# Performance work log

Hardware: AMD Instinct MI355X
Metric: run time of the kernel (lower is better)

The kernel has to match this reference:

```python
import jax, jax.numpy as jnp
import numpy as np

N, E, D, H, L, G, OUT = 100000, 1600000, 64, 64, 3, 128, 10
BN_EPS = 1e-5

def setup_inputs() -> dict:
    key = jax.random.key(0)
    ks = jax.random.split(key, 8)
    x = jax.random.normal(ks[0], (N, D), dtype=jnp.float32)
    edge_index = jax.random.randint(ks[1], (2, E), 0, N, dtype=jnp.int64)
    batch = jnp.sort(jax.random.randint(ks[2], (N,), 0, G, dtype=jnp.int64))
    W1 = jax.random.normal(ks[3], (L, D, H), dtype=jnp.float32) / np.sqrt(D)
    b1 = jnp.zeros((L, H), dtype=jnp.float32)
    gamma = jnp.ones((L, H), dtype=jnp.float32)
    beta = jnp.zeros((L, H), dtype=jnp.float32)
    W2 = jax.random.normal(ks[4], (L, H, H), dtype=jnp.float32) / np.sqrt(H)
    b2 = jnp.zeros((L, H), dtype=jnp.float32)
    Wout = jax.random.normal(ks[5], (L, H, OUT), dtype=jnp.float32) / np.sqrt(H)
    bout = jnp.zeros((L, OUT), dtype=jnp.float32)
    return {"x": x, "edge_index": edge_index, "batch": batch, "W1": W1, "b1": b1,
            "gamma": gamma, "beta": beta, "W2": W2, "b2": b2, "Wout": Wout, "bout": bout}

def _gin_layer(x, src, dst, W1, b1, g, bt, W2, b2):
    # GIN sum aggregation, eps = 0: (1+eps)*x + sum_{j->i} x_j
    agg = x + jax.ops.segment_sum(x[src], dst, num_segments=x.shape[0])
    h = agg @ W1 + b1
    mu = jnp.mean(h, axis=0)
    var = jnp.var(h, axis=0)
    h = (h - mu) * jax.lax.rsqrt(var + BN_EPS) * g + bt  # BatchNorm1d (batch stats)
    h = jax.nn.relu(h)
    return h @ W2 + b2

def reference(x, edge_index, batch, W1, b1, gamma, beta, W2, b2, Wout, bout):
    src, dst = edge_index[0], edge_index[1]
    score = jnp.zeros((G, OUT), dtype=x.dtype)
    for l in range(L):
        x = _gin_layer(x, src, dst, W1[l], b1[l], gamma[l], beta[l], W2[l], b2[l])
        pooled = jax.ops.segment_sum(x, batch, num_segments=G)  # global_add_pool
        score = score + (pooled @ Wout[l] + bout[l])  # dropout is identity in eval
    return score
```

## Files before the change

kernel.cpp:

```cpp
#include <hip/hip_runtime.h>

typedef unsigned int uint;

#define N_NODES 100000
#define E_EDGES 1600000
#define L_LAYERS 3
#define G_GRAPHS 128
#define OUT_F 10
#define BN_EPS 1e-5f

#define BSHIFT 7
#define NSTRIPE ((N_NODES + 127) >> 7)
#define CHUNK 2048
#define NCHUNK ((E_EDGES + CHUNK - 1) / CHUNK)
#define PAD8(d) (((d) + 7) & ~7)
#define BCAP (2048 * 103)
#define FB_GRID (103 * 8)
#define SCAP 2560
#define SNBR 3584

__device__ __forceinline__ uint bf_pack(float a, float b) {
    uint ua = __float_as_uint(a);
    ua = (ua + 0x7fffu + ((ua >> 16) & 1u)) >> 16;
    uint ub = __float_as_uint(b);
    ub = (ub + 0x7fffu + ((ub >> 16) & 1u)) >> 16;
    return ua | (ub << 16);
}
__device__ __forceinline__ unsigned short bf1(float a) {
    uint ua = __float_as_uint(a);
    return (unsigned short)((ua + 0x7fffu + ((ua >> 16) & 1u)) >> 16);
}
__device__ __forceinline__ float lo16(uint u) { return __uint_as_float(u << 16); }
__device__ __forceinline__ float hi16(uint u) { return __uint_as_float(u & 0xffff0000u); }

__global__ __launch_bounds__(256) void init_kernel(int* __restrict__ gcur,
                                                   int* __restrict__ scur) {
    int t = blockIdx.x * 256 + threadIdx.x;
    if (t < 8) gcur[t] = t * BCAP;
    if (t < NSTRIPE) scur[t] = t * SCAP;
}

__global__ __launch_bounds__(256) void fillA_kernel(
    const int* __restrict__ src, const int* __restrict__ dst,
    int* __restrict__ gcur, int2* __restrict__ epair) {
    __shared__ int lcnt[8];
    __shared__ int lbase[8];
    int tid = threadIdx.x;
    int base = blockIdx.x * CHUNK;
    if (tid < 8) lcnt[tid] = 0;
    __syncthreads();

    int sd[8], ss[8], bk[8], off[8];
    #pragma unroll
    for (int it = 0; it < 8; ++it) {
        int e = base + it * 256 + tid;
        bk[it] = -1;
        if (e < E_EDGES) {
            sd[it] = dst[e];
            ss[it] = src[e];
            bk[it] = (sd[it] >> BSHIFT) & 7;
            off[it] = atomicAdd(&lcnt[bk[it]], 1);
        }
    }
    __syncthreads();
    if (tid < 8) lbase[tid] = atomicAdd(&gcur[tid], lcnt[tid]);
    __syncthreads();
    #pragma unroll
    for (int it = 0; it < 8; ++it) {
        if (bk[it] >= 0)
            epair[lbase[bk[it]] + off[it]] = make_int2(ss[it], sd[it]);
    }
}

__global__ __launch_bounds__(256) void fillB2_kernel(
    const int2* __restrict__ epair1, const int* __restrict__ gcur,
    int* __restrict__ scur, int2* __restrict__ epair2) {
    __shared__ int lcnt[98];
    __shared__ int lbase[98];
    int tid = threadIdx.x;
    int g = blockIdx.x & 7;
    int c = blockIdx.x >> 3;
    int ebeg = g * BCAP + c * CHUNK;
    int eend = gcur[g];
    if (tid < 98) lcnt[tid] = 0;
    __syncthreads();

    int2 pp[8]; int bk[8], off[8];
    #pragma unroll
    for (int it = 0; it < 8; ++it) {
        int i = ebeg + it * 256 + tid;
        bk[it] = -1;
        if (i < eend) {
            pp[it] = epair1[i];
            bk[it] = pp[it].y >> 10;
            off[it] = atomicAdd(&lcnt[bk[it]], 1);
        }
    }
    __syncthreads();
    if (tid < 98 && lcnt[tid] > 0)
        lbase[tid] = atomicAdd(&scur[(tid << 3) | g], lcnt[tid]);
    __syncthreads();
    #pragma unroll
    for (int it = 0; it < 8; ++it) {
        if (bk[it] >= 0)
            epair2[lbase[bk[it]] + off[it]] = pp[it];
    }
}

__global__ __launch_bounds__(256) void fillC2_kernel(
    const int2* __restrict__ epair2, const int* __restrict__ scur,
    int* __restrict__ rbeg, int* __restrict__ rend, int* __restrict__ nbr) {
    __shared__ int cnt[128];
    __shared__ int loc[128];
    __shared__ int off[128];
    __shared__ int buf[SNBR];
    __shared__ int stotal;
    int s = blockIdx.x;
    int tid = threadIdx.x;
    int node0 = s << 7;
    int qbeg = s * SCAP;
    int qend = scur[s];
    if (tid < 128) cnt[tid] = 0;
    __syncthreads();

    for (int i = qbeg + tid; i < qend; i += 256)
        atomicAdd(&cnt[epair2[i].y & 127], 1);
    __syncthreads();

    int v = (tid < 128) ? PAD8(cnt[tid]) : 0;
    if (tid < 128) loc[tid] = v;
    __syncthreads();
    for (int o = 1; o < 128; o <<= 1) {
        int u = (tid < 128 && tid >= o) ? loc[tid - o] : 0;
        __syncthreads();
        if (tid < 128) loc[tid] += u;
        __syncthreads();
    }
    int sbase = s * SNBR;
    if (tid < 128) {
        int ex = loc[tid] - v;
        off[tid] = ex;
        int node = node0 + tid;
        if (node < N_NODES) {
            rbeg[node] = sbase + ex;
            rend[node] = sbase + ex + v;
        }
    }
    if (tid == 0) stotal = loc[127];
    __syncthreads();
    int total = stotal;

    for (int i = tid; i < total; i += 256) buf[i] = N_NODES;
    __syncthreads();

    for (int i = qbeg + tid; i < qend; i += 256) {
        int2 p = epair2[i];
        int pos = atomicAdd(&off[p.y & 127], 1);
        buf[pos] = p.x;
    }
    __syncthreads();

    for (int i = tid * 4; i < total; i += 1024)
        *reinterpret_cast<int4*>(nbr + sbase + i) = *reinterpret_cast<const int4*>(buf + i);
}

__global__ __launch_bounds__(256) void tobf_kernel(const float* __restrict__ x,
                                                   uint* __restrict__ xbf) {
    int i = blockIdx.x * 256 + threadIdx.x;
    if (i < N_NODES * 8) {
        float4 a = reinterpret_cast<const float4*>(x)[i * 2];
        float4 b = reinterpret_cast<const float4*>(x)[i * 2 + 1];
        uint4 o;
        o.x = bf_pack(a.x, a.y);
        o.y = bf_pack(a.z, a.w);
        o.z = bf_pack(b.x, b.y);
        o.w = bf_pack(b.z, b.w);
        reinterpret_cast<uint4*>(xbf)[i] = o;
    }
    if (i < 8) reinterpret_cast<uint4*>(xbf)[N_NODES * 8 + i] = make_uint4(0, 0, 0, 0);
}

__global__ __launch_bounds__(256) void gemm1_fused_kernel(
    const uint* __restrict__ xbf, const int* __restrict__ rbeg,
    const int* __restrict__ rend, const int* __restrict__ nbr,
    const float* __restrict__ W1, const float* __restrict__ b1,
    unsigned short* __restrict__ h16, float* __restrict__ stats) {
    __shared__ float sA[64][68];
    __shared__ unsigned short sWh[64][64];
    int tid = threadIdx.x;
    int row0 = blockIdx.x * 64;

    for (int i = tid; i < 1024; i += 256) {
        float4 w = reinterpret_cast<const float4*>(W1)[i];
        unsigned short* p = &sWh[0][0] + i * 4;
        p[0] = bf1(w.x); p[1] = bf1(w.y); p[2] = bf1(w.z); p[3] = bf1(w.w);
    }

    const uint4* xb4 = reinterpret_cast<const uint4*>(xbf);
    int c8 = tid & 7;
    int rslot = tid >> 3;
    for (int rr = 0; rr < 2; ++rr) {
        int r = rslot + 32 * rr;
        int gr = row0 + r;
        float a0 = 0.f, a1 = 0.f, a2 = 0.f, a3 = 0.f;
        float a4 = 0.f, a5 = 0.f, a6 = 0.f, a7 = 0.f;
        if (gr < N_NODES) {
            uint4 sv = xb4[(size_t)gr * 8 + c8];
            a0 = lo16(sv.x); a1 = hi16(sv.x); a2 = lo16(sv.y); a3 = hi16(sv.y);
            a4 = lo16(sv.z); a5 = hi16(sv.z); a6 = lo16(sv.w); a7 = hi16(sv.w);
            int beg = rbeg[gr], end = rend[gr];
            int4 ia = *reinterpret_cast<const int4*>(nbr + beg);
            int4 ib = *reinterpret_cast<const int4*>(nbr + beg + 4);
            for (int j = beg; j < end; j += 8) {
                int4 ian = *reinterpret_cast<const int4*>(nbr + j + 8);
                int4 ibn = *reinterpret_cast<const int4*>(nbr + j + 12);
                uint4 v0 = xb4[(size_t)ia.x * 8 + c8];
                uint4 v1 = xb4[(size_t)ia.y * 8 + c8];
                uint4 v2 = xb4[(size_t)ia.z * 8 + c8];
                uint4 v3 = xb4[(size_t)ia.w * 8 + c8];
                uint4 v4 = xb4[(size_t)ib.x * 8 + c8];
                uint4 v5 = xb4[(size_t)ib.y * 8 + c8];
                uint4 v6 = xb4[(size_t)ib.z * 8 + c8];
                uint4 v7 = xb4[(size_t)ib.w * 8 + c8];
                a0 += lo16(v0.x); a1 += hi16(v0.x); a2 += lo16(v0.y); a3 += hi16(v0.y);
                a4 += lo16(v0.z); a5 += hi16(v0.z); a6 += lo16(v0.w); a7 += hi16(v0.w);
                a0 += lo16(v1.x); a1 += hi16(v1.x); a2 += lo16(v1.y); a3 += hi16(v1.y);
                a4 += lo16(v1.z); a5 += hi16(v1.z); a6 += lo16(v1.w); a7 += hi16(v1.w);
                a0 += lo16(v2.x); a1 += hi16(v2.x); a2 += lo16(v2.y); a3 += hi16(v2.y);
                a4 += lo16(v2.z); a5 += hi16(v2.z); a6 += lo16(v2.w); a7 += hi16(v2.w);
                a0 += lo16(v3.x); a1 += hi16(v3.x); a2 += lo16(v3.y); a3 += hi16(v3.y);
                a4 += lo16(v3.z); a5 += hi16(v3.z); a6 += lo16(v3.w); a7 += hi16(v3.w);
                a0 += lo16(v4.x); a1 += hi16(v4.x); a2 += lo16(v4.y); a3 += hi16(v4.y);
                a4 += lo16(v4.z); a5 += hi16(v4.z); a6 += lo16(v4.w); a7 += hi16(v4.w);
                a0 += lo16(v5.x); a1 += hi16(v5.x); a2 += lo16(v5.y); a3 += hi16(v5.y);
                a4 += lo16(v5.z); a5 += hi16(v5.z); a6 += lo16(v5.w); a7 += hi16(v5.w);
                a0 += lo16(v6.x); a1 += hi16(v6.x); a2 += lo16(v6.y); a3 += hi16(v6.y);
                a4 += lo16(v6.z); a5 += hi16(v6.z); a6 += lo16(v6.w); a7 += hi16(v6.w);
                a0 += lo16(v7.x); a1 += hi16(v7.x); a2 += lo16(v7.y); a3 += hi16(v7.y);
                a4 += lo16(v7.z); a5 += hi16(v7.z); a6 += lo16(v7.w); a7 += hi16(v7.w);
                ia = ian; ib = ibn;
            }
        }
        *reinterpret_cast<float4*>(&sA[r][c8 * 8])     = make_float4(a0, a1, a2, a3);
        *reinterpret_cast<float4*>(&sA[r][c8 * 8 + 4]) = make_float4(a4, a5, a6, a7);
    }
    __syncthreads();

    int ct = tid & 15, rt = tid >> 4;
    int cbase = ct * 4, rbase = rt * 4;
    float4 bias = reinterpret_cast<const float4*>(b1)[ct];
    float acc[4][4];
    #pragma unroll
    for (int i = 0; i < 4; ++i) {
        acc[i][0] = bias.x; acc[i][1] = bias.y; acc[i][2] = bias.z; acc[i][3] = bias.w;
    }
    for (int k = 0; k < 64; ++k) {
        float A0 = sA[rbase + 0][k], A1 = sA[rbase + 1][k];
        float A2 = sA[rbase + 2][k], A3 = sA[rbase + 3][k];
        uint2 wp = *reinterpret_cast<const uint2*>(&sWh[k][cbase]);
        float w0 = lo16(wp.x), w1 = hi16(wp.x), w2 = lo16(wp.y), w3 = hi16(wp.y);
        acc[0][0] = fmaf(A0, w0, acc[0][0]); acc[0][1] = fmaf(A0, w1, acc[0][1]);
        acc[0][2] = fmaf(A0, w2, acc[0][2]); acc[0][3] = fmaf(A0, w3, acc[0][3]);
        acc[1][0] = fmaf(A1, w0, acc[1][0]); acc[1][1] = fmaf(A1, w1, acc[1][1]);
        acc[1][2] = fmaf(A1, w2, acc[1][2]); acc[1][3] = fmaf(A1, w3, acc[1][3]);
        acc[2][0] = fmaf(A2, w0, acc[2][0]); acc[2][1] = fmaf(A2, w1, acc[2][1]);
        acc[2][2] = fmaf(A2, w2, acc[2][2]); acc[2][3] = fmaf(A2, w3, acc[2][3]);
        acc[3][0] = fmaf(A3, w0, acc[3][0]); acc[3][1] = fmaf(A3, w1, acc[3][1]);
        acc[3][2] = fmaf(A3, w2, acc[3][2]); acc[3][3] = fmaf(A3, w3, acc[3][3]);
    }

    float csum[4] = {0.f, 0.f, 0.f, 0.f};
    float csq[4]  = {0.f, 0.f, 0.f, 0.f};
    #pragma unroll
    for (int i = 0; i < 4; ++i) {
        int gr = row0 + rbase + i;
        if (gr < N_NODES) {
            uint2 o;
            o.x = bf_pack(acc[i][0], acc[i][1]);
            o.y = bf_pack(acc[i][2], acc[i][3]);
            *reinterpret_cast<uint2*>(&h16[(size_t)gr * 64 + cbase]) = o;
            #pragma unroll
            for (int j = 0; j < 4; ++j) {
                csum[j] += acc[i][j];
                csq[j]  += acc[i][j] * acc[i][j];
            }
        }
    }
    __syncthreads();
    float* scratch = &sA[0][0];
    #pragma unroll
    for (int j = 0; j < 4; ++j) {
        scratch[rt * 136 + cbase + j]      = csum[j];
        scratch[rt * 136 + 64 + cbase + j] = csq[j];
    }
    __syncthreads();
    if (tid < 64) {
        float s = 0.f, q = 0.f;
        #pragma unroll
        for (int r2 = 0; r2 < 16; ++r2) {
            s += scratch[r2 * 136 + tid];
            q += scratch[r2 * 136 + 64 + tid];
        }
        unsafeAtomicAdd(&stats[tid], s);
        unsafeAtomicAdd(&stats[64 + tid], q);
    }
}

__global__ __launch_bounds__(256) void gemm2_pool_kernel(
    const unsigned short* __restrict__ h16, const float* __restrict__ stats,
    const float* __restrict__ gamma, const float* __restrict__ beta,
    const float* __restrict__ W2, const float* __restrict__ b2,
    const int* __restrict__ batch, float* __restrict__ pooled,
    unsigned short* __restrict__ xout) {
    __shared__ float sA[64][68];
    __shared__ unsigned short sWh[64][64];
    int tid = threadIdx.x;
    int row0 = blockIdx.x * 64;

    for (int i = tid; i < 1024; i += 256) {
        float4 w = reinterpret_cast<const float4*>(W2)[i];
        unsigned short* p = &sWh[0][0] + i * 4;
        p[0] = bf1(w.x); p[1] = bf1(w.y); p[2] = bf1(w.z); p[3] = bf1(w.w);
    }

    int c8 = tid & 7;
    float scv[8], shv[8];
    #pragma unroll
    for (int k = 0; k < 8; ++k) {
        int col = c8 * 8 + k;
        float mu = stats[col] * (1.0f / N_NODES);
        float var = stats[64 + col] * (1.0f / N_NODES) - mu * mu;
        scv[k] = gamma[col] * rsqrtf(var + BN_EPS);
        shv[k] = beta[col] - mu * scv[k];
    }

    const uint4* h4 = reinterpret_cast<const uint4*>(h16);
    for (int i = tid; i < 512; i += 256) {
        int r = i >> 3;
        int gr = row0 + r;
        float o[8] = {0.f, 0.f, 0.f, 0.f, 0.f, 0.f, 0.f, 0.f};
        if (gr < N_NODES) {
            uint4 v = h4[(size_t)gr * 8 + c8];
            float f[8] = {lo16(v.x), hi16(v.x), lo16(v.y), hi16(v.y),
                          lo16(v.z), hi16(v.z), lo16(v.w), hi16(v.w)};
            #pragma unroll
            for (int k = 0; k < 8; ++k)
                o[k] = fmaxf(fmaf(f[k], scv[k], shv[k]), 0.f);
        }
        *reinterpret_cast<float4*>(&sA[r][c8 * 8]) = make_float4(o[0], o[1], o[2], o[3]);
        *reinterpret_cast<float4*>(&sA[r][c8 * 8 + 4]) = make_float4(o[4], o[5], o[6], o[7]);
    }
    __syncthreads();

    int ct = tid & 15, rt = tid >> 4;
    int cbase = ct * 4, rbase = rt * 4;
    float4 bias = reinterpret_cast<const float4*>(b2)[ct];
    float acc[4][4];
    #pragma unroll
    for (int i = 0; i < 4; ++i) {
        acc[i][0] = bias.x; acc[i][1] = bias.y; acc[i][2] = bias.z; acc[i][3] = bias.w;
    }
    for (int k = 0; k < 64; ++k) {
        float A0 = sA[rbase + 0][k], A1 = sA[rbase + 1][k];
        float A2 = sA[rbase + 2][k], A3 = sA[rbase + 3][k];
        uint2 wp = *reinterpret_cast<const uint2*>(&sWh[k][cbase]);
        float w0 = lo16(wp.x), w1 = hi16(wp.x), w2 = lo16(wp.y), w3 = hi16(wp.y);
        acc[0][0] = fmaf(A0, w0, acc[0][0]); acc[0][1] = fmaf(A0, w1, acc[0][1]);
        acc[0][2] = fmaf(A0, w2, acc[0][2]); acc[0][3] = fmaf(A0, w3, acc[0][3]);
        acc[1][0] = fmaf(A1, w0, acc[1][0]); acc[1][1] = fmaf(A1, w1, acc[1][1]);
        acc[1][2] = fmaf(A1, w2, acc[1][2]); acc[1][3] = fmaf(A1, w3, acc[1][3]);
        acc[2][0] = fmaf(A2, w0, acc[2][0]); acc[2][1] = fmaf(A2, w1, acc[2][1]);
        acc[2][2] = fmaf(A2, w2, acc[2][2]); acc[2][3] = fmaf(A2, w3, acc[2][3]);
        acc[3][0] = fmaf(A3, w0, acc[3][0]); acc[3][1] = fmaf(A3, w1, acc[3][1]);
        acc[3][2] = fmaf(A3, w2, acc[3][2]); acc[3][3] = fmaf(A3, w3, acc[3][3]);
    }

    #pragma unroll
    for (int i = 0; i < 4; ++i) {
        int gr = row0 + rbase + i;
        if (gr < N_NODES) {
            uint2 o;
            o.x = bf_pack(acc[i][0], acc[i][1]);
            o.y = bf_pack(acc[i][2], acc[i][3]);
            *reinterpret_cast<uint2*>(&xout[(size_t)gr * 64 + cbase]) = o;
        }
    }

    int lastrow = row0 + 63; if (lastrow >= N_NODES) lastrow = N_NODES - 1;
    int b0 = batch[row0], bL = batch[lastrow];
    if (b0 == bL) {
        float psum[4] = {0.f, 0.f, 0.f, 0.f};
        #pragma unroll
        for (int i = 0; i < 4; ++i) {
            int gr = row0 + rbase + i;
            if (gr < N_NODES) {
                #pragma unroll
                for (int j = 0; j < 4; ++j) psum[j] += acc[i][j];
            }
        }
        __syncthreads();
        float* scratch = &sA[0][0];
        #pragma unroll
        for (int j = 0; j < 4; ++j) scratch[rt * 68 + cbase + j] = psum[j];
        __syncthreads();
        if (tid < 64) {
            float s = 0.f;
            #pragma unroll
            for (int r2 = 0; r2 < 16; ++r2) s += scratch[r2 * 68 + tid];
            unsafeAtomicAdd(&pooled[b0 * 64 + tid], s);
        }
    } else {
        #pragma unroll
        for (int j = 0; j < 4; ++j) {
            float pacc = 0.f;
            int curb = -1;
            #pragma unroll
            for (int i = 0; i < 4; ++i) {
                int gr = row0 + rbase + i;
                if (gr < N_NODES) {
                    int b = batch[gr];
                    if (b != curb) {
                        if (curb >= 0) unsafeAtomicAdd(&pooled[curb * 64 + cbase + j], pacc);
                        curb = b;
                        pacc = 0.f;
                    }
                    pacc += acc[i][j];
                }
            }
            if (curb >= 0) unsafeAtomicAdd(&pooled[curb * 64 + cbase + j], pacc);
        }
    }
}

__global__ void out_kernel(const float* __restrict__ pooled,
                           const float* __restrict__ Wout,
                           const float* __restrict__ bout,
                           float* __restrict__ score) {
    int idx = blockIdx.x * blockDim.x + threadIdx.x;
    if (idx >= G_GRAPHS * OUT_F) return;
    int g = idx / OUT_F;
    int o = idx - g * OUT_F;
    float acc = bout[o];
    #pragma unroll
    for (int k = 0; k < 64; ++k) acc += pooled[g * 64 + k] * Wout[k * OUT_F + o];
    score[idx] += acc;
}

extern "C" void kernel_launch(void* const* d_in, const int* in_sizes, int n_in,
                              void* d_out, int out_size, void* d_ws, size_t ws_size,
                              hipStream_t stream) {
    const float* x     = (const float*)d_in[0];
    const int*   ei    = (const int*)d_in[1];
    const int*   batch = (const int*)d_in[2];
    const float* W1    = (const float*)d_in[3];
    const float* b1    = (const float*)d_in[4];
    const float* gamma = (const float*)d_in[5];
    const float* beta  = (const float*)d_in[6];
    const float* W2    = (const float*)d_in[7];
    const float* b2    = (const float*)d_in[8];
    const float* Wout  = (const float*)d_in[9];
    const float* bout  = (const float*)d_in[10];
    float* out = (float*)d_out;

    unsigned short* H16 = (unsigned short*)d_ws;
    uint*  XBF    = (uint*)(H16 + (size_t)N_NODES * 64);
    float* stats  = (float*)(XBF + (size_t)(N_NODES + 1) * 32);
    float* pooled = stats + 128;
    int*   gcur   = (int*)(pooled + (size_t)G_GRAPHS * 64);
    int*   scur   = gcur + 8;
    int*   rbeg   = scur + 784;
    int*   rend   = rbeg + N_NODES;
    int*   nbr    = rend + N_NODES;
    int2*  epair1 = (int2*)(nbr + (size_t)NSTRIPE * SNBR + 16);
    int2*  epair2 = epair1 + (size_t)8 * BCAP;

    const int* src = ei;
    const int* dst = ei + E_EDGES;

    (void)hipMemsetAsync(d_out, 0, (size_t)G_GRAPHS * OUT_F * sizeof(float), stream);

    init_kernel<<<(NSTRIPE + 255) / 256, 256, 0, stream>>>(gcur, scur);
    fillA_kernel<<<NCHUNK, 256, 0, stream>>>(src, dst, gcur, epair1);
    fillB2_kernel<<<FB_GRID, 256, 0, stream>>>(epair1, gcur, scur, epair2);
    fillC2_kernel<<<NSTRIPE, 256, 0, stream>>>(epair2, scur, rbeg, rend, nbr);
    tobf_kernel<<<(N_NODES * 8 + 255) / 256, 256, 0, stream>>>(x, XBF);

    int nb = (N_NODES + 63) / 64;

    for (int l = 0; l < L_LAYERS; ++l) {
        (void)hipMemsetAsync(stats, 0, (128 + (size_t)G_GRAPHS * 64) * sizeof(float), stream);

        gemm1_fused_kernel<<<nb, 256, 0, stream>>>(XBF, rbeg, rend, nbr,
            W1 + l * 64 * 64, b1 + l * 64, H16, stats);
        gemm2_pool_kernel<<<nb, 256, 0, stream>>>(H16, stats,
            gamma + l * 64, beta + l * 64, W2 + l * 64 * 64, b2 + l * 64, batch,
            pooled, (unsigned short*)XBF);
        out_kernel<<<(G_GRAPHS * OUT_F + 127) / 128, 128, 0, stream>>>(
            pooled, Wout + l * 64 * OUT_F, bout + l * OUT_F, out);
    }
}
```

Measured before the change: 355.1 us.

## Use bf16 MFMA for the dense 64x64 GEMMs in gemm1 and gemm2 kernels

Replaces the scalar FMA 4x4 register-tiled GEMM in both fused kernels with __builtin_amdgcn_mfma_f32_16x16x32_bf16. The A tile is now stored as bf16 in shared memory and the weights are stored transposed so each wave can load 8-element k fragments. The epilogues (bf16 stores, batchnorm statistics, pooling atomics) are remapped to the MFMA output layout. This cuts ALU time for the GEMM phase and shrinks LDS use, but it rounds the aggregated activations to bf16 before the multiply and the output stores become 2-byte scattered writes.

```diff
diff --git a/kernel.cpp b/kernel.cpp
--- a/kernel.cpp
+++ b/kernel.cpp
@@ -1,6 +1,8 @@
 #include <hip/hip_runtime.h>
 
 typedef unsigned int uint;
+typedef short bf16x8 __attribute__((ext_vector_type(8)));
+typedef float f32x4 __attribute__((ext_vector_type(4)));
 
 #define N_NODES 100000
 #define E_EDGES 1600000
@@ -185,15 +187,18 @@
     const int* __restrict__ rend, const int* __restrict__ nbr,
     const float* __restrict__ W1, const float* __restrict__ b1,
     unsigned short* __restrict__ h16, float* __restrict__ stats) {
-    __shared__ float sA[64][68];
-    __shared__ unsigned short sWh[64][64];
+    __shared__ unsigned short sA[64][72];
+    __shared__ unsigned short sW[64][72];
     int tid = threadIdx.x;
     int row0 = blockIdx.x * 64;
 
     for (int i = tid; i < 1024; i += 256) {
+        int k = i >> 4, cb = (i & 15) * 4;
         float4 w = reinterpret_cast<const float4*>(W1)[i];
-        unsigned short* p = &sWh[0][0] + i * 4;
-        p[0] = bf1(w.x); p[1] = bf1(w.y); p[2] = bf1(w.z); p[3] = bf1(w.w);
+        sW[cb + 0][k] = bf1(w.x);
+        sW[cb + 1][k] = bf1(w.y);
+        sW[cb + 2][k] = bf1(w.z);
+        sW[cb + 3][k] = bf1(w.w);
     }
 
     const uint4* xb4 = reinterpret_cast<const uint4*>(xbf);
@@ -241,65 +246,63 @@
                 ia = ian; ib = ibn;
             }
         }
-        *reinterpret_cast<float4*>(&sA[r][c8 * 8])     = make_float4(a0, a1, a2, a3);
-        *reinterpret_cast<float4*>(&sA[r][c8 * 8 + 4]) = make_float4(a4, a5, a6, a7);
-    }
-    __syncthreads();
-
-    int ct = tid & 15, rt = tid >> 4;
-    int cbase = ct * 4, rbase = rt * 4;
-    float4 bias = reinterpret_cast<const float4*>(b1)[ct];
-    float acc[4][4];
-    #pragma unroll
-    for (int i = 0; i < 4; ++i) {
-        acc[i][0] = bias.x; acc[i][1] = bias.y; acc[i][2] = bias.z; acc[i][3] = bias.w;
-    }
-    for (int k = 0; k < 64; ++k) {
-        float A0 = sA[rbase + 0][k], A1 = sA[rbase + 1][k];
-        float A2 = sA[rbase + 2][k], A3 = sA[rbase + 3][k];
-        uint2 wp = *reinterpret_cast<const uint2*>(&sWh[k][cbase]);
-        float w0 = lo16(wp.x), w1 = hi16(wp.x), w2 = lo16(wp.y), w3 = hi16(wp.y);
-        acc[0][0] = fmaf(A0, w0, acc[0][0]); acc[0][1] = fmaf(A0, w1, acc[0][1]);
-        acc[0][2] = fmaf(A0, w2, acc[0][2]); acc[0][3] = fmaf(A0, w3, acc[0][3]);
-        acc[1][0] = fmaf(A1, w0, acc[1][0]); acc[1][1] = fmaf(A1, w1, acc[1][1]);
-        acc[1][2] = fmaf(A1, w2, acc[1][2]); acc[1][3] = fmaf(A1, w3, acc[1][3]);
-        acc[2][0] = fmaf(A2, w0, acc[2][0]); acc[2][1] = fmaf(A2, w1, acc[2][1]);
-        acc[2][2] = fmaf(A2, w2, acc[2][2]); acc[2][3] = fmaf(A2, w3, acc[2][3]);
-        acc[3][0] = fmaf(A3, w0, acc[3][0]); acc[3][1] = fmaf(A3, w1, acc[3][1]);
-        acc[3][2] = fmaf(A3, w2, acc[3][2]); acc[3][3] = fmaf(A3, w3, acc[3][3]);
-    }
-
-    float csum[4] = {0.f, 0.f, 0.f, 0.f};
-    float csq[4]  = {0.f, 0.f, 0.f, 0.f};
-    #pragma unroll
-    for (int i = 0; i < 4; ++i) {
-        int gr = row0 + rbase + i;
-        if (gr < N_NODES) {
-            uint2 o;
-            o.x = bf_pack(acc[i][0], acc[i][1]);
-            o.y = bf_pack(acc[i][2], acc[i][3]);
-            *reinterpret_cast<uint2*>(&h16[(size_t)gr * 64 + cbase]) = o;
-            #pragma unroll
-            for (int j = 0; j < 4; ++j) {
-                csum[j] += acc[i][j];
-                csq[j]  += acc[i][j] * acc[i][j];
+        uint4 o;
+        o.x = bf_pack(a0, a1); o.y = bf_pack(a2, a3);
+        o.z = bf_pack(a4, a5); o.w = bf_pack(a6, a7);
+        *reinterpret_cast<uint4*>(&sA[r][c8 * 8]) = o;
+    }
+    __syncthreads();
+
+    int w = tid >> 6;
+    int l = tid & 63;
+    int lr = l & 15;
+    int lk = l >> 4;
+    f32x4 acc[4];
+    #pragma unroll
+    for (int ct = 0; ct < 4; ++ct) {
+        float b = b1[ct * 16 + lr];
+        acc[ct] = (f32x4){b, b, b, b};
+    }
+    #pragma unroll
+    for (int ct = 0; ct < 4; ++ct) {
+        #pragma unroll
+        for (int kc = 0; kc < 2; ++kc) {
+            bf16x8 av = *reinterpret_cast<const bf16x8*>(&sA[w * 16 + lr][kc * 32 + lk * 8]);
+            bf16x8 bv = *reinterpret_cast<const bf16x8*>(&sW[ct * 16 + lr][kc * 32 + lk * 8]);
+            acc[ct] = __builtin_amdgcn_mfma_f32_16x16x32_bf16(av, bv, acc[ct], 0, 0, 0);
+        }
+    }
+
+    float s4[4] = {0.f, 0.f, 0.f, 0.f};
+    float q4[4] = {0.f, 0.f, 0.f, 0.f};
+    #pragma unroll
+    for (int ct = 0; ct < 4; ++ct) {
+        #pragma unroll
+        for (int r = 0; r < 4; ++r) {
+            int row = row0 + w * 16 + lk * 4 + r;
+            float v = acc[ct][r];
+            if (row < N_NODES) {
+                h16[(size_t)row * 64 + ct * 16 + lr] = bf1(v);
+                s4[ct] += v;
+                q4[ct] += v * v;
             }
         }
     }
     __syncthreads();
-    float* scratch = &sA[0][0];
-    #pragma unroll
-    for (int j = 0; j < 4; ++j) {
-        scratch[rt * 136 + cbase + j]      = csum[j];
-        scratch[rt * 136 + 64 + cbase + j] = csq[j];
+    float* scr = reinterpret_cast<float*>(&sW[0][0]);
+    int g16 = w * 4 + lk;
+    #pragma unroll
+    for (int ct = 0; ct < 4; ++ct) {
+        scr[g16 * 64 + ct * 16 + lr] = s4[ct];
+        scr[1024 + g16 * 64 + ct * 16 + lr] = q4[ct];
     }
     __syncthreads();
     if (tid < 64) {
         float s = 0.f, q = 0.f;
         #pragma unroll
         for (int r2 = 0; r2 < 16; ++r2) {
-            s += scratch[r2 * 136 + tid];
-            q += scratch[r2 * 136 + 64 + tid];
+            s += scr[r2 * 64 + tid];
+            q += scr[1024 + r2 * 64 + tid];
         }
         unsafeAtomicAdd(&stats[tid], s);
         unsafeAtomicAdd(&stats[64 + tid], q);
@@ -312,15 +315,18 @@
     const float* __restrict__ W2, const float* __restrict__ b2,
     const int* __restrict__ batch, float* __restrict__ pooled,
     unsigned short* __restrict__ xout) {
-    __shared__ float sA[64][68];
-    __shared__ unsigned short sWh[64][64];
+    __shared__ unsigned short sA[64][72];
+    __shared__ unsigned short sW[64][72];
     int tid = threadIdx.x;
     int row0 = blockIdx.x * 64;
 
     for (int i = tid; i < 1024; i += 256) {
+        int k = i >> 4, cb = (i & 15) * 4;
         float4 w = reinterpret_cast<const float4*>(W2)[i];
-        unsigned short* p = &sWh[0][0] + i * 4;
-        p[0] = bf1(w.x); p[1] = bf1(w.y); p[2] = bf1(w.z); p[3] = bf1(w.w);
+        sW[cb + 0][k] = bf1(w.x);
+        sW[cb + 1][k] = bf1(w.y);
+        sW[cb + 2][k] = bf1(w.z);
+        sW[cb + 3][k] = bf1(w.w);
     }
 
     int c8 = tid & 7;
@@ -347,87 +353,88 @@
             for (int k = 0; k < 8; ++k)
                 o[k] = fmaxf(fmaf(f[k], scv[k], shv[k]), 0.f);
         }
-        *reinterpret_cast<float4*>(&sA[r][c8 * 8]) = make_float4(o[0], o[1], o[2], o[3]);
-        *reinterpret_cast<float4*>(&sA[r][c8 * 8 + 4]) = make_float4(o[4], o[5], o[6], o[7]);
-    }
-    __syncthreads();
-
-    int ct = tid & 15, rt = tid >> 4;
-    int cbase = ct * 4, rbase = rt * 4;
-    float4 bias = reinterpret_cast<const float4*>(b2)[ct];
-    float acc[4][4];
-    #pragma unroll
-    for (int i = 0; i < 4; ++i) {
-        acc[i][0] = bias.x; acc[i][1] = bias.y; acc[i][2] = bias.z; acc[i][3] = bias.w;
-    }
-    for (int k = 0; k < 64; ++k) {
-        float A0 = sA[rbase + 0][k], A1 = sA[rbase + 1][k];
-        float A2 = sA[rbase + 2][k], A3 = sA[rbase + 3][k];
-        uint2 wp = *reinterpret_cast<const uint2*>(&sWh[k][cbase]);
-        float w0 = lo16(wp.x), w1 = hi16(wp.x), w2 = lo16(wp.y), w3 = hi16(wp.y);
-        acc[0][0] = fmaf(A0, w0, acc[0][0]); acc[0][1] = fmaf(A0, w1, acc[0][1]);
-        acc[0][2] = fmaf(A0, w2, acc[0][2]); acc[0][3] = fmaf(A0, w3, acc[0][3]);
-        acc[1][0] = fmaf(A1, w0, acc[1][0]); acc[1][1] = fmaf(A1, w1, acc[1][1]);
-        acc[1][2] = fmaf(A1, w2, acc[1][2]); acc[1][3] = fmaf(A1, w3, acc[1][3]);
-        acc[2][0] = fmaf(A2, w0, acc[2][0]); acc[2][1] = fmaf(A2, w1, acc[2][1]);
-        acc[2][2] = fmaf(A2, w2, acc[2][2]); acc[2][3] = fmaf(A2, w3, acc[2][3]);
-        acc[3][0] = fmaf(A3, w0, acc[3][0]); acc[3][1] = fmaf(A3, w1, acc[3][1]);
-        acc[3][2] = fmaf(A3, w2, acc[3][2]); acc[3][3] = fmaf(A3, w3, acc[3][3]);
-    }
-
-    #pragma unroll
-    for (int i = 0; i < 4; ++i) {
-        int gr = row0 + rbase + i;
-        if (gr < N_NODES) {
-            uint2 o;
-            o.x = bf_pack(acc[i][0], acc[i][1]);
-            o.y = bf_pack(acc[i][2], acc[i][3]);
-            *reinterpret_cast<uint2*>(&xout[(size_t)gr * 64 + cbase]) = o;
+        uint4 p;
+        p.x = bf_pack(o[0], o[1]); p.y = bf_pack(o[2], o[3]);
+        p.z = bf_pack(o[4], o[5]); p.w = bf_pack(o[6], o[7]);
+        *reinterpret_cast<uint4*>(&sA[r][c8 * 8]) = p;
+    }
+    __syncthreads();
+
+    int w = tid >> 6;
+    int l = tid & 63;
+    int lr = l & 15;
+    int lk = l >> 4;
+    f32x4 acc[4];
+    #pragma unroll
+    for (int ct = 0; ct < 4; ++ct) {
+        float b = b2[ct * 16 + lr];
+        acc[ct] = (f32x4){b, b, b, b};
+    }
+    #pragma unroll
+    for (int ct = 0; ct < 4; ++ct) {
+        #pragma unroll
+        for (int kc = 0; kc < 2; ++kc) {
+            bf16x8 av = *reinterpret_cast<const bf16x8*>(&sA[w * 16 + lr][kc * 32 + lk * 8]);
+            bf16x8 bv = *reinterpret_cast<const bf16x8*>(&sW[ct * 16 + lr][kc * 32 + lk * 8]);
+            acc[ct] = __builtin_amdgcn_mfma_f32_16x16x32_bf16(av, bv, acc[ct], 0, 0, 0);
+        }
+    }
+
+    #pragma unroll
+    for (int ct = 0; ct < 4; ++ct) {
+        #pragma unroll
+        for (int r = 0; r < 4; ++r) {
+            int row = row0 + w * 16 + lk * 4 + r;
+            if (row < N_NODES)
+                xout[(size_t)row * 64 + ct * 16 + lr] = bf1(acc[ct][r]);
         }
     }
 
     int lastrow = row0 + 63; if (lastrow >= N_NODES) lastrow = N_NODES - 1;
     int b0 = batch[row0], bL = batch[lastrow];
     if (b0 == bL) {
-        float psum[4] = {0.f, 0.f, 0.f, 0.f};
-        #pragma unroll
-        for (int i = 0; i < 4; ++i) {
-            int gr = row0 + rbase + i;
-            if (gr < N_NODES) {
-                #pragma unroll
-                for (int j = 0; j < 4; ++j) psum[j] += acc[i][j];
+        float ps[4] = {0.f, 0.f, 0.f, 0.f};
+        #pragma unroll
+        for (int ct = 0; ct < 4; ++ct) {
+            #pragma unroll
+            for (int r = 0; r < 4; ++r) {
+                int row = row0 + w * 16 + lk * 4 + r;
+                if (row < N_NODES) ps[ct] += acc[ct][r];
             }
         }
         __syncthreads();
-        float* scratch = &sA[0][0];
-        #pragma unroll
-        for (int j = 0; j < 4; ++j) scratch[rt * 68 + cbase + j] = psum[j];
+        float* scr = reinterpret_cast<float*>(&sW[0][0]);
+        int g16 = w * 4 + lk;
+        #pragma unroll
+        for (int ct = 0; ct < 4; ++ct)
+            scr[g16 * 64 + ct * 16 + lr] = ps[ct];
         __syncthreads();
         if (tid < 64) {
             float s = 0.f;
             #pragma unroll
-            for (int r2 = 0; r2 < 16; ++r2) s += scratch[r2 * 68 + tid];
+            for (int r2 = 0; r2 < 16; ++r2) s += scr[r2 * 64 + tid];
             unsafeAtomicAdd(&pooled[b0 * 64 + tid], s);
         }
     } else {
         #pragma unroll
-        for (int j = 0; j < 4; ++j) {
+        for (int ct = 0; ct < 4; ++ct) {
             float pacc = 0.f;
             int curb = -1;
+            int col = ct * 16 + lr;
             #pragma unroll
-            for (int i = 0; i < 4; ++i) {
-                int gr = row0 + rbase + i;
-                if (gr < N_NODES) {
-                    int b = batch[gr];
+            for (int r = 0; r < 4; ++r) {
+                int row = row0 + w * 16 + lk * 4 + r;
+                if (row < N_NODES) {
+                    int b = batch[row];
                     if (b != curb) {
-                        if (curb >= 0) unsafeAtomicAdd(&pooled[curb * 64 + cbase + j], pacc);
+                        if (curb >= 0) unsafeAtomicAdd(&pooled[curb * 64 + col], pacc);
                         curb = b;
                         pacc = 0.f;
                     }
-                    pacc += acc[i][j];
+                    pacc += acc[ct][r];
                 }
             }
-            if (curb >= 0) unsafeAtomicAdd(&pooled[curb * 64 + cbase + j], pacc);
+            if (curb >= 0) unsafeAtomicAdd(&pooled[curb * 64 + col], pacc);
         }
     }
 }
```

Result: faster. 316.3 us (-10.9%).
